# Optimization experiments

Hardware: AMD Instinct MI355X
Metric: run time of the kernel (lower is better)

## Reference

```python
import jax, jax.numpy as jnp
import numpy as np

B, TENC, EPROJS, DUNITS, ODIM, L, ATT_DIM = 64, 800, 512, 512, 5000, 128, 320
SOS = EOS = ODIM - 1


def setup_inputs() -> dict:
    key = jax.random.key(0)
    ks = jax.random.split(key, 16)
    s = 0.02
    D = DUNITS
    return {
        "hpad": jax.random.normal(ks[0], (B, TENC, EPROJS), jnp.float32),
        # keep lengths in [TENC//2, TENC] so every row has valid frames
        "hlen": jnp.clip(jax.random.randint(ks[1], (B,), 0, TENC + 1), TENC // 2, TENC).astype(jnp.int32),
        "ys": jax.random.randint(ks[2], (B, L), 0, ODIM - 1),  # int labels (exclude eos)
        "embed": s * jax.random.normal(ks[3], (ODIM, D), jnp.float32),
        # torch.nn.LSTMCell params: gates order (i, f, g, o)
        "W_ih0": s * jax.random.normal(ks[4], (4 * D, D + EPROJS), jnp.float32),
        "W_hh0": s * jax.random.normal(ks[5], (4 * D, D), jnp.float32),
        "b_ih0": jnp.zeros((4 * D,), jnp.float32),
        "b_hh0": jnp.zeros((4 * D,), jnp.float32),
        "W_ih1": s * jax.random.normal(ks[6], (4 * D, D), jnp.float32),
        "W_hh1": s * jax.random.normal(ks[7], (4 * D, D), jnp.float32),
        "b_ih1": jnp.zeros((4 * D,), jnp.float32),
        "b_hh1": jnp.zeros((4 * D,), jnp.float32),
        # AttDot attention projections (no bias, as in espnet mlp_enc/mlp_dec usage)
        "Wa_enc": s * jax.random.normal(ks[8], (EPROJS, ATT_DIM), jnp.float32),
        "Wa_dec": s * jax.random.normal(ks[9], (D, ATT_DIM), jnp.float32),
        "W_out": s * jax.random.normal(ks[10], (ODIM, D), jnp.float32),
        "b_out": jnp.zeros((ODIM,), jnp.float32),
    }


def _lstm_cell(x, h, c, Wi, Wh, bi, bh):
    g = x @ Wi.T + bi + h @ Wh.T + bh
    i, f, gg, o = jnp.split(g, 4, axis=-1)
    c2 = jax.nn.sigmoid(f) * c + jax.nn.sigmoid(i) * jnp.tanh(gg)
    h2 = jax.nn.sigmoid(o) * jnp.tanh(c2)
    return h2, c2


def _forward(hpad, hlen, ys, embed, W_ih0, W_hh0, b_ih0, b_hh0,
             W_ih1, W_hh1, b_ih1, b_hh1, Wa_enc, Wa_dec, W_out, b_out):
    D = DUNITS
    tmask = jnp.arange(TENC)[None, :] < hlen[:, None]          # [B, T]
    hm = hpad * tmask[:, :, None]                               # mask_by_length
    enc_pre = jnp.tanh(jnp.einsum('bte,ea->bta', hm, Wa_enc))   # [B, T, A] precomputed

    sos_col = jnp.full((B, 1), SOS, ys.dtype)
    eos_col = jnp.full((B, 1), EOS, ys.dtype)
    ys_in = jnp.concatenate([sos_col, ys], axis=1)              # [B, L+1]
    ys_out = jnp.concatenate([ys, eos_col], axis=1)             # [B, L+1]
    eys = embed[ys_in]                                          # [B, L+1, D]

    zeros = jnp.zeros((B, D), hpad.dtype)
    carry0 = (zeros, zeros, zeros, zeros)  # z0, c0, z1, c1

    def step(carry, ey_t):
        z0, c0, z1, c1 = carry
        # AttDot: e = <tanh(enc W), tanh(z0 W)> with length masking
        d = jnp.tanh(z0 @ Wa_dec)                               # [B, A]
        e = jnp.einsum('ba,bta->bt', d, enc_pre)                # [B, T]
        e = jnp.where(tmask, e, jnp.float32(-1e9))
        w = jax.nn.softmax(e, axis=-1)
        att_c = jnp.einsum('bt,bte->be', w, hm)                 # [B, eprojs]
        x = jnp.concatenate([ey_t, att_c], axis=-1)             # [B, D+eprojs]
        z0, c0 = _lstm_cell(x, z0, c0, W_ih0, W_hh0, b_ih0, b_hh0)
        z1, c1 = _lstm_cell(z0, z1, c1, W_ih1, W_hh1, b_ih1, b_hh1)
        return (z0, c0, z1, c1), z1                             # gen_feat='s' -> top hidden

    _, z_all = jax.lax.scan(step, carry0, jnp.swapaxes(eys, 0, 1))  # [L+1, B, D]
    z_all = jnp.swapaxes(z_all, 0, 1)                           # [B, L+1, D]

    logits = jnp.einsum('bld,vd->blv', z_all, W_out) + b_out    # [B, L+1, V]
    logp = jax.nn.log_softmax(logits, axis=-1)
    nll = -jnp.take_along_axis(logp, ys_out[..., None], axis=-1)[..., 0]
    # F.cross_entropy mean over all tokens (no padding here), then *= mean(len(ys_in)) - 1 = L
    loss = nll.mean() * jnp.float32(L)
    acc = (logits.argmax(-1) == ys_out).mean()
    return loss, acc


def reference(hpad, hlen, ys, embed, W_ih0, W_hh0, b_ih0, b_hh0,
              W_ih1, W_hh1, b_ih1, b_hh1, Wa_enc, Wa_dec, W_out, b_out):
    return _forward(hpad, hlen, ys, embed, W_ih0, W_hh0, b_ih0, b_hh0,
                    W_ih1, W_hh1, b_ih1, b_hh1, Wa_enc, Wa_dec, W_out, b_out)
```

## Files before the change

### kernel.cpp

```cpp
#include <hip/hip_runtime.h>
#include <math.h>

typedef unsigned short u16;
typedef float f32x4 __attribute__((ext_vector_type(4)));
typedef short s16x8 __attribute__((ext_vector_type(8)));

#define ODIM 5000
#define NROWS 8256

__device__ inline u16 f2bf(float f){
  unsigned u = __float_as_uint(f);
  return (u16)((u + 0x7FFFu + ((u >> 16) & 1u)) >> 16);
}
__device__ inline float bf2f(u16 h){ return __uint_as_float(((unsigned)h) << 16); }
__device__ inline float sigm(float x){ return 1.f/(1.f + expf(-x)); }

__global__ void a0_init(float* att2, float* pd, float* z0f, float* z1f,
                        float* c0, float* c1, float* accum){
  int tid = blockIdx.x*256 + threadIdx.x, n = 64*256;
  for (int i=tid;i<2*64*516;i+=n) att2[i]=0.f;
  for (int i=tid;i<655360;i+=n) pd[i]=0.f;
  for (int i=tid;i<32768;i+=n){ z0f[i]=0.f; z1f[i]=0.f; c0[i]=0.f; c1[i]=0.f; }
  if (tid < 8) accum[tid]=0.f;
}

__global__ void a1_wcvt(const float* waenc, const float* wadec,
  const float* wih0, const float* whh0, const float* wih1, const float* whh1,
  const float* bih0, const float* bhh0, const float* bih1, const float* bhh1,
  const float* wout,
  u16* waencT, u16* wdKC, u16* wcat0, u16* wcat1, u16* wee, u16* woutb,
  float* bc0, float* bc1)
{
  int tid = blockIdx.x*blockDim.x + threadIdx.x;
  int nth = gridDim.x*blockDim.x;
  for (int i=tid; i<320*512; i+=nth){
    int n=i>>9, k=i&511;
    waencT[i] = f2bf(waenc[k*320+n]);
    wdKC[i]   = f2bf(wadec[i]);
  }
  for (int i=tid; i<2048*1024; i+=nth){
    int np=i>>10, k=i&1023;
    int u=np>>2, g=np&3, r=g*512+u;
    wcat0[i] = f2bf(k<512 ? wih0[r*1024+512+k] : whh0[r*512+(k-512)]);
    wcat1[i] = f2bf(k<512 ? wih1[r*512+k]      : whh1[r*512+(k-512)]);
  }
  for (int i=tid; i<2048*512; i+=nth){
    int np=i>>9, k=i&511;
    int u=np>>2, g=np&3, r=g*512+u;
    wee[i] = f2bf(wih0[r*1024+k]);
  }
  for (int i=tid; i<5000*512; i+=nth) woutb[i] = f2bf(wout[i]);
  for (int i=tid; i<2048; i+=nth){
    int u=i>>2, g=i&3, r=g*512+u;
    bc0[i] = bih0[r]+bhh0[r];
    bc1[i] = bih1[r]+bhh1[r];
  }
}

__global__ __launch_bounds__(256) void a2_encpre(
  const float* __restrict__ hpad, const int* __restrict__ hlen,
  const u16* __restrict__ waencT, u16* __restrict__ hm, u16* __restrict__ encp)
{
  __shared__ u16 A[64][40];
  __shared__ u16 BT[320][40];
  int tid = threadIdx.x, blk = blockIdx.x;
  int wave = tid>>6, lane = tid&63;
  f32x4 acc[20];
  #pragma unroll
  for (int f=0;f<20;f++) acc[f] = (f32x4){0.f,0.f,0.f,0.f};
  int srow = tid>>2, skoff = (tid&3)*8;
  int grow_s = blk*64 + srow;
  int b_s = grow_s/800, t_s = grow_s - b_s*800;
  bool valid_s = t_s < hlen[b_s];
  for (int c=0;c<16;c++){
    int k0 = c*32;
    {
      const float* src = hpad + (size_t)grow_s*512 + k0 + skoff;
      float4 v0 = *(const float4*)(src);
      float4 v1 = *(const float4*)(src+4);
      if (!valid_s){ v0 = make_float4(0,0,0,0); v1 = make_float4(0,0,0,0); }
      short4 p0 = make_short4((short)f2bf(v0.x),(short)f2bf(v0.y),(short)f2bf(v0.z),(short)f2bf(v0.w));
      short4 p1 = make_short4((short)f2bf(v1.x),(short)f2bf(v1.y),(short)f2bf(v1.z),(short)f2bf(v1.w));
      *(short4*)&A[srow][skoff]   = p0;
      *(short4*)&A[srow][skoff+4] = p1;
      *(short4*)(hm + (size_t)grow_s*512 + k0 + skoff)     = p0;
      *(short4*)(hm + (size_t)grow_s*512 + k0 + skoff + 4) = p1;
    }
    for (int id=tid; id<1280; id+=256){
      int n = id>>2, kv = (id&3)*8;
      *(s16x8*)&BT[n][kv] = *(const s16x8*)(waencT + n*512 + k0 + kv);
    }
    __syncthreads();
    s16x8 av = *(const s16x8*)&A[wave*16 + (lane&15)][(lane>>4)*8];
    #pragma unroll
    for (int f=0;f<20;f++){
      s16x8 bv = *(const s16x8*)&BT[f*16+(lane&15)][(lane>>4)*8];
      acc[f] = __builtin_amdgcn_mfma_f32_16x16x32_bf16(av,bv,acc[f],0,0,0);
    }
    __syncthreads();
  }
  #pragma unroll
  for (int f=0;f<20;f++){
    int col = f*16 + (lane&15);
    #pragma unroll
    for (int r=0;r<4;r++){
      int grow = blk*64 + wave*16 + (lane>>4)*4 + r;
      encp[(size_t)grow*320 + col] = f2bf(tanhf(acc[f][r]));
    }
  }
}

__global__ __launch_bounds__(256) void a3_geys(
  const int* __restrict__ ys, const float* __restrict__ embed,
  const u16* __restrict__ wee, const float* __restrict__ bc0,
  u16* __restrict__ geys)
{
  __shared__ u16 A[64][88];
  __shared__ u16 BT[256][88];
  int t = blockIdx.x, nt = blockIdx.y, tid = threadIdx.x;
  int wave=tid>>6, lane=tid&63;
  f32x4 acc[16];
  #pragma unroll
  for (int f=0;f<16;f++) acc[f]=(f32x4){0.f,0.f,0.f,0.f};
  int srow = tid>>2, skoff=(tid&3)*16;
  int idx = (t==0) ? (ODIM-1) : ys[srow*128 + (t-1)];
  const float* asrc = embed + (size_t)idx*512;
  for (int c=0;c<8;c++){
    int k0=c*64;
    #pragma unroll
    for (int i=0;i<16;i+=4){
      float4 v = *(const float4*)(asrc + k0 + skoff + i);
      *(short4*)&A[srow][skoff+i] =
        make_short4((short)f2bf(v.x),(short)f2bf(v.y),(short)f2bf(v.z),(short)f2bf(v.w));
    }
    for (int id=tid; id<2048; id+=256){
      int n = id>>3, kv=(id&7)*8;
      *(s16x8*)&BT[n][kv] = *(const s16x8*)(wee + (size_t)(nt*256+n)*512 + k0 + kv);
    }
    __syncthreads();
    #pragma unroll
    for (int kk=0;kk<64;kk+=32){
      s16x8 av = *(const s16x8*)&A[wave*16+(lane&15)][kk+(lane>>4)*8];
      #pragma unroll
      for (int f=0;f<16;f++){
        s16x8 bv = *(const s16x8*)&BT[f*16+(lane&15)][kk+(lane>>4)*8];
        acc[f] = __builtin_amdgcn_mfma_f32_16x16x32_bf16(av,bv,acc[f],0,0,0);
      }
    }
    __syncthreads();
  }
  #pragma unroll
  for (int f=0;f<16;f++){
    int colL = f*16+(lane&15);
    int gc = nt*256+colL;
    float bb = bc0[gc];
    #pragma unroll
    for (int r=0;r<4;r++){
      int row = wave*16 + (lane>>4)*4 + r;
      geys[(size_t)(t*64+row)*2048 + gc] = f2bf(acc[f][r] + bb);
    }
  }
}

__global__ __launch_bounds__(256) void k1p(
  int t,
  const u16* __restrict__ encp, const u16* __restrict__ hm, const int* __restrict__ hlen,
  const u16* __restrict__ pd,
  const u16* __restrict__ wcat1, const float* __restrict__ bc1,
  const u16* __restrict__ z0b, u16* __restrict__ z1b, float* __restrict__ c1,
  u16* __restrict__ zall, float* __restrict__ att)
{
  __shared__ __align__(16) char smem[42240];
  const int blk = blockIdx.x, tid = threadIdx.x;
  const int wave = tid>>6, lane = tid&63;
  const int p2 = (t+1)&1;

  if (blk < 512){
    int b = blk>>3, ch = blk&7;
    float* attp = att + ((t&1)*64*516);
    u16*  pdl  = (u16*)smem;
    float* dl  = (float*)(smem+40960);
    float* attl = (float*)smem;
    float* sl  = (float*)(smem+8192);
    for (int id=tid; id<2560; id+=256){
      int s = id/40, c8 = (id - s*40)*8;
      *(s16x8*)&pdl[s*320+c8] = *(const s16x8*)(pd + (size_t)s*20480 + b*320 + c8);
    }
    __syncthreads();
    for (int col=tid; col<320; col+=256){
      float a0=0.f,a1=0.f,a2=0.f,a3=0.f;
      #pragma unroll
      for (int s=0;s<64;s+=4){
        a0 += bf2f(pdl[s*320+col]);
        a1 += bf2f(pdl[(s+1)*320+col]);
        a2 += bf2f(pdl[(s+2)*320+col]);
        a3 += bf2f(pdl[(s+3)*320+col]);
      }
      dl[col] = tanhf((a0+a1)+(a2+a3));
    }
    __syncthreads();
    float dreg[8];
    #pragma unroll
    for (int j=0;j<8;j++) dreg[j] = (lane<40) ? dl[lane*8+j] : 0.f;
    float attacc[8];
    #pragma unroll
    for (int j=0;j<8;j++) attacc[j]=0.f;
    float sacc = 0.f;
    int len = hlen[b];
    int t0 = ch*100;
    int tend = t0+100 < len ? t0+100 : len;
    for (int i0 = t0 + wave; i0 < tend; i0 += 16){
      s16x8 ev[4], hv[4];
      #pragma unroll
      for (int q=0;q<4;q++){
        int tt = i0 + 4*q;
        if (tt < tend){
          if (lane<40) ev[q] = *(const s16x8*)(encp + (size_t)(b*800+tt)*320 + lane*8);
          hv[q] = *(const s16x8*)(hm + (size_t)(b*800+tt)*512 + lane*8);
        }
      }
      #pragma unroll
      for (int q=0;q<4;q++){
        int tt = i0 + 4*q;
        if (tt < tend){
          float e = 0.f;
          if (lane<40){
            #pragma unroll
            for (int j=0;j<8;j++) e += dreg[j]*bf2f((u16)ev[q][j]);
          }
          #pragma unroll
          for (int off=32; off; off>>=1) e += __shfl_xor(e, off);
          float pw = expf(fminf(e, 60.f));
          sacc += pw;
          #pragma unroll
          for (int j=0;j<8;j++) attacc[j] += pw*bf2f((u16)hv[q][j]);
        }
      }
    }
    __syncthreads();
    #pragma unroll
    for (int j=0;j<8;j++) attl[wave*512 + lane*8+j] = attacc[j];
    if (lane==0) sl[wave] = sacc;
    __syncthreads();
    for (int c2 = tid; c2 < 512; c2 += 256){
      float v = attl[c2]+attl[512+c2]+attl[1024+c2]+attl[1536+c2];
      atomicAdd(&attp[b*516 + c2], v);
    }
    if (tid==0) atomicAdd(&attp[b*516 + 512], sl[0]+sl[1]+sl[2]+sl[3]);
  } else {
    if (t < 1) return;
    int nb = blk - 512;
    const u16* z0n = z0b + p2*64*512;
    const u16* z1p = z1b + ((p2^1)*64*512);
    u16* z1n = z1b + p2*64*512;
    u16* zallt = zall + (size_t)(t-1)*64*512;
    u16 (*A)[88]  = (u16(*)[88])smem;
    u16 (*BT)[88] = (u16(*)[88])(smem+11264);
    f32x4 acc[2];
    acc[0]=(f32x4){0.f,0.f,0.f,0.f}; acc[1]=(f32x4){0.f,0.f,0.f,0.f};
    int srow=tid>>2, skoff=(tid&3)*16;
    int brow=tid>>3, bkoff=(tid&7)*8;
    for (int c=0;c<16;c++){
      int k0=c*64;
      const u16* asrc = (c<8) ? (z0n + srow*512 + k0 + skoff)
                              : (z1p + srow*512 + (k0-512) + skoff);
      *(s16x8*)&A[srow][skoff]   = *(const s16x8*)asrc;
      *(s16x8*)&A[srow][skoff+8] = *(const s16x8*)(asrc+8);
      *(s16x8*)&BT[brow][bkoff] = *(const s16x8*)(wcat1 + (size_t)(nb*32+brow)*1024 + k0 + bkoff);
      __syncthreads();
      #pragma unroll
      for (int kk=0;kk<64;kk+=32){
        s16x8 av = *(const s16x8*)&A[wave*16+(lane&15)][kk+(lane>>4)*8];
        #pragma unroll
        for (int f=0;f<2;f++){
          s16x8 bv = *(const s16x8*)&BT[f*16+(lane&15)][kk+(lane>>4)*8];
          acc[f] = __builtin_amdgcn_mfma_f32_16x16x32_bf16(av,bv,acc[f],0,0,0);
        }
      }
      __syncthreads();
    }
    float (*gl)[36] = (float(*)[36])smem;
    #pragma unroll
    for (int f=0;f<2;f++){
      int colL = f*16+(lane&15);
      float bb = bc1[nb*32+colL];
      #pragma unroll
      for (int r=0;r<4;r++){
        int rowL = wave*16+(lane>>4)*4+r;
        gl[rowL][colL] = acc[f][r] + bb;
      }
    }
    __syncthreads();
    for (int it=tid; it<512; it+=256){
      int bb=it>>3, ul=it&7;
      float gi=gl[bb][ul*4], gf=gl[bb][ul*4+1], gg=gl[bb][ul*4+2], go=gl[bb][ul*4+3];
      int ug = nb*8+ul;
      float cp = c1[bb*512+ug];
      float cn = sigm(gf)*cp + sigm(gi)*tanhf(gg);
      float z = sigm(go)*tanhf(cn);
      c1[bb*512+ug]=cn;
      u16 zb = f2bf(z);
      z1n[bb*512+ug]=zb;
      zallt[bb*512+ug]=zb;
    }
  }
}

__global__ __launch_bounds__(256) void k2p(
  const float* __restrict__ attp, float* __restrict__ attz,
  const u16* __restrict__ z0p, u16* __restrict__ z0n,
  float* __restrict__ c0,
  const u16* __restrict__ wcat0, const u16* __restrict__ geyt,
  const u16* __restrict__ wdKC, u16* __restrict__ pdout)
{
  __shared__ __align__(16) char smem[16896];
  __shared__ float sinv[64];
  __shared__ float zsl[512];
  __shared__ u16 wsl[2560];
  u16 (*A)[88]  = (u16(*)[88])smem;
  u16 (*BT)[88] = (u16(*)[88])(smem+11264);
  int tid = threadIdx.x, nb = blockIdx.x;
  int wave=tid>>6, lane=tid&63;
  if (tid < 64) sinv[tid] = 1.f/attp[tid*516+512];
  for (int id=tid; id<320; id+=256)
    *(s16x8*)&wsl[id*8] = *(const s16x8*)(wdKC + (size_t)nb*2560 + id*8);
  __syncthreads();
  f32x4 acc[2];
  acc[0]=(f32x4){0.f,0.f,0.f,0.f}; acc[1]=(f32x4){0.f,0.f,0.f,0.f};
  int srow=tid>>2, skoff=(tid&3)*16;
  int brow=tid>>3, bkoff=(tid&7)*8;
  for (int c=0;c<16;c++){
    int k0=c*64;
    if (c<8){
      const float* src = attp + srow*516 + k0 + skoff;
      float sv = sinv[srow];
      #pragma unroll
      for (int i=0;i<16;i+=4){
        float4 v = *(const float4*)(src+i);
        *(short4*)&A[srow][skoff+i] = make_short4(
          (short)f2bf(v.x*sv),(short)f2bf(v.y*sv),(short)f2bf(v.z*sv),(short)f2bf(v.w*sv));
      }
    } else {
      const u16* src = z0p + srow*512 + (k0-512) + skoff;
      *(s16x8*)&A[srow][skoff]   = *(const s16x8*)(src);
      *(s16x8*)&A[srow][skoff+8] = *(const s16x8*)(src+8);
    }
    *(s16x8*)&BT[brow][bkoff] = *(const s16x8*)(wcat0 + (size_t)(nb*32+brow)*1024 + k0 + bkoff);
    __syncthreads();
    #pragma unroll
    for (int kk=0;kk<64;kk+=32){
      s16x8 av = *(const s16x8*)&A[wave*16+(lane&15)][kk+(lane>>4)*8];
      #pragma unroll
      for (int f=0;f<2;f++){
        s16x8 bv = *(const s16x8*)&BT[f*16+(lane&15)][kk+(lane>>4)*8];
        acc[f] = __builtin_amdgcn_mfma_f32_16x16x32_bf16(av,bv,acc[f],0,0,0);
      }
    }
    __syncthreads();
  }
  float (*gl)[36] = (float(*)[36])smem;
  #pragma unroll
  for (int f=0;f<2;f++){
    int colL = f*16+(lane&15);
    #pragma unroll
    for (int r=0;r<4;r++){
      int rowL = wave*16+(lane>>4)*4+r;
      gl[rowL][colL] = acc[f][r] + bf2f(geyt[rowL*2048 + nb*32 + colL]);
    }
  }
  __syncthreads();
  for (int it=tid; it<512; it+=256){
    int bb=it>>3, ul=it&7;
    float gi=gl[bb][ul*4], gf=gl[bb][ul*4+1], gg=gl[bb][ul*4+2], go=gl[bb][ul*4+3];
    int ug = nb*8+ul;
    float cp = c0[bb*512+ug];
    float cn = sigm(gf)*cp + sigm(gi)*tanhf(gg);
    float z = sigm(go)*tanhf(cn);
    c0[bb*512+ug]=cn;
    z0n[bb*512+ug]=f2bf(z);
    zsl[it] = z;
  }
  __syncthreads();
  for (int idx=tid; idx<20480; idx+=256){
    int b = idx/320, col = idx - b*320;
    float a = 0.f;
    #pragma unroll
    for (int ul=0; ul<8; ul++)
      a += zsl[b*8+ul]*bf2f(wsl[ul*320+col]);
    pdout[(size_t)nb*20480 + idx] = f2bf(a);
  }
  for (int i=tid + nb*256; i < 64*516; i += 64*256) attz[i] = 0.f;
}

__global__ __launch_bounds__(256) void kf_cell1(
  const u16* __restrict__ z0n, const u16* __restrict__ z1p,
  u16* __restrict__ z1n, float* __restrict__ c1,
  const u16* __restrict__ wcat1, const float* __restrict__ bc1,
  u16* __restrict__ zallt)
{
  __shared__ __align__(16) char smem[25600];
  int tid = threadIdx.x, wave=tid>>6, lane=tid&63;
  int nb = blockIdx.x;
  u16 (*A)[88]  = (u16(*)[88])smem;
  u16 (*BT)[88] = (u16(*)[88])(smem+11264);
  f32x4 acc[2];
  acc[0]=(f32x4){0.f,0.f,0.f,0.f}; acc[1]=(f32x4){0.f,0.f,0.f,0.f};
  int srow=tid>>2, skoff=(tid&3)*16;
  int brow=tid>>3, bkoff=(tid&7)*8;
  for (int c=0;c<16;c++){
    int k0=c*64;
    const u16* asrc = (c<8) ? (z0n + srow*512 + k0 + skoff)
                            : (z1p + srow*512 + (k0-512) + skoff);
    *(s16x8*)&A[srow][skoff]   = *(const s16x8*)asrc;
    *(s16x8*)&A[srow][skoff+8] = *(const s16x8*)(asrc+8);
    *(s16x8*)&BT[brow][bkoff] = *(const s16x8*)(wcat1 + (size_t)(nb*32+brow)*1024 + k0 + bkoff);
    __syncthreads();
    #pragma unroll
    for (int kk=0;kk<64;kk+=32){
      s16x8 av = *(const s16x8*)&A[wave*16+(lane&15)][kk+(lane>>4)*8];
      #pragma unroll
      for (int f=0;f<2;f++){
        s16x8 bv = *(const s16x8*)&BT[f*16+(lane&15)][kk+(lane>>4)*8];
        acc[f] = __builtin_amdgcn_mfma_f32_16x16x32_bf16(av,bv,acc[f],0,0,0);
      }
    }
    __syncthreads();
  }
  float (*gl)[36] = (float(*)[36])smem;
  #pragma unroll
  for (int f=0;f<2;f++){
    int colL = f*16+(lane&15);
    float bb = bc1[nb*32+colL];
    #pragma unroll
    for (int r=0;r<4;r++){
      int rowL = wave*16+(lane>>4)*4+r;
      gl[rowL][colL] = acc[f][r] + bb;
    }
  }
  __syncthreads();
  for (int it=tid; it<512; it+=256){
    int bb=it>>3, ul=it&7;
    float gi=gl[bb][ul*4], gf=gl[bb][ul*4+1], gg=gl[bb][ul*4+2], go=gl[bb][ul*4+3];
    int ug = nb*8+ul;
    float cp = c1[bb*512+ug];
    float cn = sigm(gf)*cp + sigm(gi)*tanhf(gg);
    float z = sigm(go)*tanhf(cn);
    c1[bb*512+ug]=cn;
    u16 zb = f2bf(z);
    z1n[bb*512+ug]=zb;
    zallt[bb*512+ug]=zb;
  }
}

__global__ __launch_bounds__(512) void k4_logits(
  const u16* __restrict__ zall, const u16* __restrict__ woutb,
  const float* __restrict__ b_out, const int* __restrict__ ys,
  float* __restrict__ partials)
{
  __shared__ char smem[46080];
  u16 (*A)[40]  = (u16(*)[40])smem;
  u16 (*BT)[40] = (u16(*)[40])(smem + 5120);
  int t = blockIdx.x, v = blockIdx.y;
  int tid = threadIdx.x, wave = tid>>6, lane = tid&63;
  int mf = wave>>1;
  int nh = (wave&1)*256;
  f32x4 acc[16];
  #pragma unroll
  for (int f=0;f<16;f++) acc[f]=(f32x4){0.f,0.f,0.f,0.f};
  for (int c=0;c<16;c++){
    int k0 = c*32;
    { int row = tid>>3, koff=(tid&7)*4;
      *(short4*)&A[row][koff] = *(const short4*)(zall + (size_t)(t*64+row)*512 + k0 + koff); }
    { int n = v*512 + tid;
      if (n < ODIM){
        const u16* src = woutb + (size_t)n*512 + k0;
        #pragma unroll
        for (int i=0;i<32;i+=8) *(s16x8*)&BT[tid][i] = *(const s16x8*)(src+i);
      } else {
        s16x8 z = 0;
        #pragma unroll
        for (int i=0;i<32;i+=8) *(s16x8*)&BT[tid][i] = z;
      }
    }
    __syncthreads();
    s16x8 av = *(const s16x8*)&A[mf*16 + (lane&15)][(lane>>4)*8];
    #pragma unroll
    for (int f=0;f<16;f++){
      s16x8 bv = *(const s16x8*)&BT[nh + f*16 + (lane&15)][(lane>>4)*8];
      acc[f] = __builtin_amdgcn_mfma_f32_16x16x32_bf16(av,bv,acc[f],0,0,0);
    }
    __syncthreads();
  }
  float (*ll)[518] = (float(*)[518])smem;
  for (int g=0; g<4; g++){
    if (mf == g){
      #pragma unroll
      for (int f=0;f<16;f++){
        int colL = nh + f*16 + (lane&15);
        int gcol = v*512 + colL;
        float bo = (gcol < ODIM) ? b_out[gcol] : 0.f;
        #pragma unroll
        for (int r=0;r<4;r++){
          int rowL = (lane>>4)*4 + r;
          ll[rowL][colL] = acc[f][r] + bo;
        }
      }
    }
    __syncthreads();
    int r = tid>>5, j = tid&31;
    float m = -1e30f, s = 0.f, amax = -1e30f; int aidx = 0;
    #pragma unroll
    for (int i=0;i<16;i++){
      int cL = j + 32*i;
      int gc = v*512 + cL;
      if (gc < ODIM){
        float val = ll[r][cL];
        if (val > m){ s = s*expf(m-val) + 1.f; m = val; }
        else s += expf(val - m);
        if (val > amax){ amax = val; aidx = gc; }
      }
    }
    #pragma unroll
    for (int off=16; off; off>>=1){
      float mo = __shfl_xor(m, off), so = __shfl_xor(s, off);
      float ao = __shfl_xor(amax, off); int io = __shfl_xor(aidx, off);
      float M = fmaxf(m, mo);
      s = s*expf(m-M) + so*expf(mo-M);
      m = M;
      if (ao > amax || (ao == amax && io < aidx)){ amax = ao; aidx = io; }
    }
    if (j == 0){
      int b = g*16 + r;
      int grow = t*64 + b;
      int lab = (t < 128) ? ys[b*128 + t] : (ODIM-1);
      float labval = 0.f, labf = 0.f;
      int lo = lab - v*512;
      if (lo >= 0 && lo < 512){ labval = ll[r][lo]; labf = 1.f; }
      float* pp = partials + (size_t)(grow*10 + v)*8;
      pp[0]=m; pp[1]=s; pp[2]=amax; pp[3]=__int_as_float(aidx); pp[4]=labval; pp[5]=labf;
    }
    __syncthreads();
  }
}

__global__ __launch_bounds__(256) void k5_loss(
  const float* __restrict__ partials, const int* __restrict__ ys, float* accum)
{
  int row = blockIdx.x*256 + threadIdx.x;
  float nll = 0.f; int corr = 0;
  if (row < NROWS){
    float M=-1e30f, S=0.f, amax=-1e30f, labval=0.f; int aidx=0;
    for (int v=0;v<10;v++){
      const float* pp = partials + (size_t)(row*10+v)*8;
      float m=pp[0], s=pp[1], a=pp[2]; int ai=__float_as_int(pp[3]);
      float MM = fmaxf(M, m);
      S = S*expf(M-MM) + s*expf(m-MM);
      M = MM;
      if (a > amax || (a == amax && ai < aidx)){ amax=a; aidx=ai; }
      if (pp[5] != 0.f) labval = pp[4];
    }
    nll = M + logf(S) - labval;
    int t = row>>6, b = row&63;
    int lab = (t < 128) ? ys[b*128+t] : (ODIM-1);
    corr = (aidx == lab) ? 1 : 0;
  }
  __shared__ float sn[256]; __shared__ int sc[256];
  sn[threadIdx.x]=nll; sc[threadIdx.x]=corr; __syncthreads();
  for (int st=128; st; st>>=1){
    if (threadIdx.x<st){ sn[threadIdx.x]+=sn[threadIdx.x+st]; sc[threadIdx.x]+=sc[threadIdx.x+st]; }
    __syncthreads();
  }
  if (threadIdx.x==0){
    atomicAdd(accum, sn[0]);
    atomicAdd((int*)accum + 1, sc[0]);
  }
}

__global__ void k6_final(const float* accum, float* out){
  out[0] = accum[0]/(float)NROWS * 128.f;
  out[1] = (float)(((const int*)accum)[1])/(float)NROWS;
}

extern "C" void kernel_launch(void* const* d_in, const int* in_sizes, int n_in,
                              void* d_out, int out_size, void* d_ws, size_t ws_size,
                              hipStream_t stream)
{
  const float* hpad  = (const float*)d_in[0];
  const int*   hlen  = (const int*)d_in[1];
  const int*   ys    = (const int*)d_in[2];
  const float* embed = (const float*)d_in[3];
  const float* wih0  = (const float*)d_in[4];
  const float* whh0  = (const float*)d_in[5];
  const float* bih0  = (const float*)d_in[6];
  const float* bhh0  = (const float*)d_in[7];
  const float* wih1  = (const float*)d_in[8];
  const float* whh1  = (const float*)d_in[9];
  const float* bih1  = (const float*)d_in[10];
  const float* bhh1  = (const float*)d_in[11];
  const float* waenc = (const float*)d_in[12];
  const float* wadec = (const float*)d_in[13];
  const float* wout  = (const float*)d_in[14];
  const float* bout  = (const float*)d_in[15];

  char* ws = (char*)d_ws;
  u16*   hm      = (u16*)(ws + 0);
  u16*   encp    = (u16*)(ws + 52428800);
  u16*   waencT  = (u16*)(ws + 85196800);
  u16*   wdKC    = (u16*)(ws + 85524480);
  u16*   wcat0   = (u16*)(ws + 85852160);
  u16*   wcat1   = (u16*)(ws + 90046464);
  u16*   wee     = (u16*)(ws + 94240768);
  u16*   woutb   = (u16*)(ws + 96337920);
  float* bc0     = (float*)(ws + 101457920);
  float* bc1     = (float*)(ws + 101466112);
  u16*   geys    = (u16*)(ws + 101474304);
  float* att     = (float*)(ws + 135331840);
  u16*   z0b     = (u16*)(ws + 135596032);
  u16*   z1b     = (u16*)(ws + 135727104);
  float* c0      = (float*)(ws + 135858176);
  float* c1      = (float*)(ws + 135989248);
  u16*   zall    = (u16*)(ws + 136120320);
  u16*   pd      = (u16*)(ws + 144574464);
  float* partials= (float*)(ws + 144574464);
  float* accum   = (float*)(ws + 147216384);

  a0_init<<<64,256,0,stream>>>(att, (float*)pd, (float*)z0b, (float*)z1b, c0, c1, accum);
  a1_wcvt<<<512,256,0,stream>>>(waenc, wadec, wih0, whh0, wih1, whh1,
                                bih0, bhh0, bih1, bhh1, wout,
                                waencT, wdKC, wcat0, wcat1, wee, woutb, bc0, bc1);
  a2_encpre<<<800,256,0,stream>>>(hpad, hlen, waencT, hm, encp);
  a3_geys<<<dim3(129,8),256,0,stream>>>(ys, embed, wee, bc0, geys);

  for (int t=0; t<129; t++){
    int p = t & 1, q = p^1;
    k1p<<<576,256,0,stream>>>(t, encp, hm, hlen, pd, wcat1, bc1,
                              z0b, z1b, c1, zall, att);
    k2p<<<64,256,0,stream>>>(att + p*64*516, att + q*64*516,
                             z0b + q*64*512, z0b + p*64*512,
                             c0, wcat0, geys + (size_t)t*64*2048,
                             wdKC, pd);
  }
  kf_cell1<<<64,256,0,stream>>>(z0b, z1b + 64*512, z1b, c1, wcat1, bc1,
                                zall + (size_t)128*64*512);

  k4_logits<<<dim3(129,10),512,0,stream>>>(zall, woutb, bout, ys, partials);
  k5_loss<<<33,256,0,stream>>>(partials, ys, accum);
  k6_final<<<1,1,0,stream>>>(accum, (float*)d_out);
}
```

Before: 6.802 ms.

## Accumulate decoder attention projection via fp32 atomics and split attention blocks finer

k2p now atomically adds its per-unit-block partial decoder projections into one fp32 accumulator instead of writing 64 bf16 partial slabs, and k1p reads the summed value directly rather than reducing 64 partials per batch row. The accumulator is double-buffered and zeroed by k1p for the next step. Attention blocks are split into 32 chunks of 25 frames per batch row for more parallelism. This adds heavy global atomic traffic and more atomics on the attention context in exchange for removing a large per-step read and reduction; it also changes summation order and precision from bf16 partials to fp32.

After: 6.602 ms. 2.9% less time.

```diff
diff --git a/kernel.cpp b/kernel.cpp
--- a/kernel.cpp
+++ b/kernel.cpp
@@ -15,11 +15,11 @@
 __device__ inline float bf2f(u16 h){ return __uint_as_float(((unsigned)h) << 16); }
 __device__ inline float sigm(float x){ return 1.f/(1.f + expf(-x)); }
 
-__global__ void a0_init(float* att2, float* pd, float* z0f, float* z1f,
+__global__ void a0_init(float* att2, float* dacc, float* z0f, float* z1f,
                         float* c0, float* c1, float* accum){
   int tid = blockIdx.x*256 + threadIdx.x, n = 64*256;
   for (int i=tid;i<2*64*516;i+=n) att2[i]=0.f;
-  for (int i=tid;i<655360;i+=n) pd[i]=0.f;
+  for (int i=tid;i<40960;i+=n) dacc[i]=0.f;
   for (int i=tid;i<32768;i+=n){ z0f[i]=0.f; z1f[i]=0.f; c0[i]=0.f; c1[i]=0.f; }
   if (tid < 8) accum[tid]=0.f;
 }
@@ -165,39 +165,25 @@
 __global__ __launch_bounds__(256) void k1p(
   int t,
   const u16* __restrict__ encp, const u16* __restrict__ hm, const int* __restrict__ hlen,
-  const u16* __restrict__ pd,
+  float* __restrict__ dacc,
   const u16* __restrict__ wcat1, const float* __restrict__ bc1,
   const u16* __restrict__ z0b, u16* __restrict__ z1b, float* __restrict__ c1,
   u16* __restrict__ zall, float* __restrict__ att)
 {
-  __shared__ __align__(16) char smem[42240];
+  __shared__ __align__(16) char smem[17408];
   const int blk = blockIdx.x, tid = threadIdx.x;
   const int wave = tid>>6, lane = tid&63;
   const int p2 = (t+1)&1;
 
-  if (blk < 512){
-    int b = blk>>3, ch = blk&7;
+  if (blk < 2048){
+    int b = blk>>5, ch = blk&31;
     float* attp = att + ((t&1)*64*516);
-    u16*  pdl  = (u16*)smem;
-    float* dl  = (float*)(smem+40960);
     float* attl = (float*)smem;
-    float* sl  = (float*)(smem+8192);
-    for (int id=tid; id<2560; id+=256){
-      int s = id/40, c8 = (id - s*40)*8;
-      *(s16x8*)&pdl[s*320+c8] = *(const s16x8*)(pd + (size_t)s*20480 + b*320 + c8);
-    }
-    __syncthreads();
-    for (int col=tid; col<320; col+=256){
-      float a0=0.f,a1=0.f,a2=0.f,a3=0.f;
-      #pragma unroll
-      for (int s=0;s<64;s+=4){
-        a0 += bf2f(pdl[s*320+col]);
-        a1 += bf2f(pdl[(s+1)*320+col]);
-        a2 += bf2f(pdl[(s+2)*320+col]);
-        a3 += bf2f(pdl[(s+3)*320+col]);
-      }
-      dl[col] = tanhf((a0+a1)+(a2+a3));
-    }
+    float* sl   = (float*)(smem+8192);
+    float* dl   = (float*)(smem+8224);
+    { int gid = blk*256 + tid;
+      if (gid < 20480) dacc[(p2^1)*20480 + gid] = 0.f; }
+    if (tid < 320) dl[tid] = tanhf(dacc[p2*20480 + b*320 + tid]);
     __syncthreads();
     float dreg[8];
     #pragma unroll
@@ -207,8 +193,8 @@
     for (int j=0;j<8;j++) attacc[j]=0.f;
     float sacc = 0.f;
     int len = hlen[b];
-    int t0 = ch*100;
-    int tend = t0+100 < len ? t0+100 : len;
+    int t0 = ch*25;
+    int tend = t0+25 < len ? t0+25 : len;
     for (int i0 = t0 + wave; i0 < tend; i0 += 16){
       s16x8 ev[4], hv[4];
       #pragma unroll
@@ -249,7 +235,7 @@
     if (tid==0) atomicAdd(&attp[b*516 + 512], sl[0]+sl[1]+sl[2]+sl[3]);
   } else {
     if (t < 1) return;
-    int nb = blk - 512;
+    int nb = blk - 2048;
     const u16* z0n = z0b + p2*64*512;
     const u16* z1p = z1b + ((p2^1)*64*512);
     u16* z1n = z1b + p2*64*512;
@@ -311,7 +297,7 @@
   const u16* __restrict__ z0p, u16* __restrict__ z0n,
   float* __restrict__ c0,
   const u16* __restrict__ wcat0, const u16* __restrict__ geyt,
-  const u16* __restrict__ wdKC, u16* __restrict__ pdout)
+  const u16* __restrict__ wdKC, float* __restrict__ dacc)
 {
   __shared__ __align__(16) char smem[16896];
   __shared__ float sinv[64];
@@ -387,7 +373,7 @@
     #pragma unroll
     for (int ul=0; ul<8; ul++)
       a += zsl[b*8+ul]*bf2f(wsl[ul*320+col]);
-    pdout[(size_t)nb*20480 + idx] = f2bf(a);
+    atomicAdd(&dacc[idx], a);
   }
   for (int i=tid + nb*256; i < 64*516; i += 64*256) attz[i] = 0.f;
 }
@@ -620,11 +606,11 @@
   float* c0      = (float*)(ws + 135858176);
   float* c1      = (float*)(ws + 135989248);
   u16*   zall    = (u16*)(ws + 136120320);
-  u16*   pd      = (u16*)(ws + 144574464);
+  float* dacc    = (float*)(ws + 144574464);
   float* partials= (float*)(ws + 144574464);
   float* accum   = (float*)(ws + 147216384);
 
-  a0_init<<<64,256,0,stream>>>(att, (float*)pd, (float*)z0b, (float*)z1b, c0, c1, accum);
+  a0_init<<<64,256,0,stream>>>(att, dacc, (float*)z0b, (float*)z1b, c0, c1, accum);
   a1_wcvt<<<512,256,0,stream>>>(waenc, wadec, wih0, whh0, wih1, whh1,
                                 bih0, bhh0, bih1, bhh1, wout,
                                 waencT, wdKC, wcat0, wcat1, wee, woutb, bc0, bc1);
@@ -633,12 +619,12 @@
 
   for (int t=0; t<129; t++){
     int p = t & 1, q = p^1;
-    k1p<<<576,256,0,stream>>>(t, encp, hm, hlen, pd, wcat1, bc1,
-                              z0b, z1b, c1, zall, att);
+    k1p<<<2112,256,0,stream>>>(t, encp, hm, hlen, dacc, wcat1, bc1,
+                               z0b, z1b, c1, zall, att);
     k2p<<<64,256,0,stream>>>(att + p*64*516, att + q*64*516,
                              z0b + q*64*512, z0b + p*64*512,
                              c0, wcat0, geys + (size_t)t*64*2048,
-                             wdKC, pd);
+                             wdKC, dacc + p*20480);
   }
   kf_cell1<<<64,256,0,stream>>>(z0b, z1b + 64*512, z1b, c1, wcat1, bc1,
                                 zall + (size_t)128*64*512);
```
